# Optimization experiments

Measured on AMD Instinct MI355X. Metric: run time of the kernel, lower is better.

The kernel has to match this reference:

```python
import jax, jax.numpy as jnp
import numpy as np

N = 50000      # nodes
E = 800000     # edges
D_IN = 128     # input_dim
D = 128        # hidden_dim
H = 8          # num_heads
DH = D // H    # head dim
S = 10         # security_feature_dim
LN_EPS = 1e-5


def setup_inputs() -> dict:
    key = jax.random.key(0)
    ks = jax.random.split(key, 16)
    def lin_w(k, fin, fout):
        return (jax.random.normal(k, (fin, fout), jnp.float32) / np.sqrt(fin)).astype(jnp.float32)
    return {
        "x": jax.random.normal(ks[0], (N, D_IN), jnp.float32),
        "edge_index": jax.random.randint(ks[1], (2, E), 0, N, jnp.int64),
        "security_features": jax.random.normal(ks[2], (N, S), jnp.float32),
        "W1": lin_w(ks[3], D_IN, D), "b1": jnp.zeros((D,), jnp.float32),
        "W2": lin_w(ks[4], D, D),    "b2": jnp.zeros((D,), jnp.float32),
        "Wq": lin_w(ks[5], D, D),    "bq": jnp.zeros((D,), jnp.float32),
        "Wk": lin_w(ks[6], D, D),    "bk": jnp.zeros((D,), jnp.float32),
        "Wv": lin_w(ks[7], D, D),    "bv": jnp.zeros((D,), jnp.float32),
        "Wsec": lin_w(ks[8], S, H),  "bsec": jnp.zeros((H,), jnp.float32),
        "Wo": lin_w(ks[9], D, D),    "bo": jnp.zeros((D,), jnp.float32),
        "ln1_g": jnp.ones((D,), jnp.float32), "ln1_b": jnp.zeros((D,), jnp.float32),
        "ln2_g": jnp.ones((D,), jnp.float32), "ln2_b": jnp.zeros((D,), jnp.float32),
    }


def _layer_norm(x, g, b):
    m = jnp.mean(x, axis=-1, keepdims=True)
    v = jnp.mean(jnp.square(x - m), axis=-1, keepdims=True)
    return (x - m) * jax.lax.rsqrt(v + LN_EPS) * g + b


def reference(x, edge_index, security_features,
              W1, b1, W2, b2, Wq, bq, Wk, bk, Wv, bv,
              Wsec, bsec, Wo, bo, ln1_g, ln1_b, ln2_g, ln2_b):
    # h = relu(linear1(x))  -- [N, D]
    h = jax.nn.relu(x @ W1 + b1)

    # SecurityAwareAttention: edge-wise multi-head attention with a
    # per-edge security bias derived from the source node's security features.
    q = (h @ Wq + bq).reshape(N, H, DH)
    k = (h @ Wk + bk).reshape(N, H, DH)
    v = (h @ Wv + bv).reshape(N, H, DH)
    src, dst = edge_index[0], edge_index[1]

    sec_bias = security_features @ Wsec + bsec            # [N, H]
    scores = jnp.einsum('ehd,ehd->eh', q[dst], k[src]) / np.sqrt(DH) + sec_bias[src]  # [E, H]

    # segment softmax over incoming edges of each destination node
    m = jax.ops.segment_max(scores, dst, num_segments=N)  # [N, H]
    e = jnp.exp(scores - m[dst])
    s = jax.ops.segment_sum(e, dst, num_segments=N)       # [N, H]
    attn = e / (s[dst] + 1e-9)                            # [E, H]

    agg = jax.ops.segment_sum(attn[:, :, None] * v[src], dst, num_segments=N)  # [N, H, DH]
    attended = agg.reshape(N, D) @ Wo + bo

    # dropout is identity (eval mode)
    out = _layer_norm(h + attended, ln1_g, ln1_b)
    out = _layer_norm(out + jax.nn.relu(out @ W2 + b2), ln2_g, ln2_b)
    return (out, attn)
```

## Files before the change

### kernel.cpp

```cpp
#include <hip/hip_runtime.h>
#include <hip/hip_bf16.h>
#include <math.h>

#define N_NODES 50000
#define N_EDGES 800000
#define DIM 128
#define NHEAD 8
#define DHEAD 16
#define SDIM 10
#define NSCAN_BLK 196

typedef __attribute__((ext_vector_type(8))) short bf16x8;
typedef __attribute__((ext_vector_type(4))) float f32x4;

__device__ __forceinline__ float bf2f(unsigned short u) {
    return __uint_as_float(((unsigned)u) << 16);
}
__device__ __forceinline__ unsigned short f2bf(float f) {
    unsigned u = __float_as_uint(f);
    return (unsigned short)((u + 0x7FFFu + ((u >> 16) & 1u)) >> 16);
}

__global__ __launch_bounds__(256) void setup_kernel(
    const float* __restrict__ W1, const float* __restrict__ Wq,
    const float* __restrict__ Wk, const float* __restrict__ Wv,
    const float* __restrict__ Wo, const float* __restrict__ W2,
    unsigned short* __restrict__ Wt, int* __restrict__ deg, int* __restrict__ ctr,
    const float* __restrict__ sec, const float* __restrict__ Wsec,
    const float* __restrict__ bsec, float* __restrict__ secb) {
    const int b = blockIdx.x, t = threadIdx.x;
    if (b < 6) {
        const float* W = (b == 0) ? W1 : (b == 1) ? Wq : (b == 2) ? Wk :
                         (b == 3) ? Wv : (b == 4) ? Wo : W2;
        unsigned short* o = Wt + b * 16384;
        for (int i = 0; i < 64; ++i) {
            int idx = t + 256 * i;
            int k = idx >> 7, n = idx & 127;
            o[n * 128 + k] = f2bf(W[idx]);
        }
    } else if (b < 202) {
        int idx = (b - 6) * 256 + t;
        if (idx < N_NODES) { deg[idx] = 0; ctr[idx] = 0; }
    } else {
        int idx = (b - 202) * 256 + t;
        if (idx < N_NODES * NHEAD) {
            int n = idx >> 3, h = idx & 7;
            float acc = bsec[h];
#pragma unroll
            for (int j = 0; j < SDIM; ++j)
                acc = fmaf(sec[n * SDIM + j], Wsec[j * NHEAD + h], acc);
            secb[idx] = acc;
        }
    }
}

__global__ __launch_bounds__(256) void count_deg_kernel(const int* __restrict__ dst,
                                                        int* __restrict__ deg) {
    int e = blockIdx.x * 256 + threadIdx.x;
    if (e < N_EDGES) atomicAdd(&deg[dst[e]], 1);
}

__global__ __launch_bounds__(256) void blocksum_kernel(const int* __restrict__ deg,
                                                       int* __restrict__ bsum) {
    const int t = threadIdx.x;
    int idx = blockIdx.x * 256 + t;
    int v = (idx < N_NODES) ? deg[idx] : 0;
#pragma unroll
    for (int m = 32; m; m >>= 1) v += __shfl_xor(v, m);
    __shared__ int ws[4];
    if ((t & 63) == 0) ws[t >> 6] = v;
    __syncthreads();
    if (t == 0) bsum[blockIdx.x] = ws[0] + ws[1] + ws[2] + ws[3];
}

__global__ __launch_bounds__(256) void scanfin2_kernel(const int* __restrict__ deg,
                                                       const int* __restrict__ bsum,
                                                       int* __restrict__ rowstart) {
    const int t = threadIdx.x, b = blockIdx.x;
    int v0 = (t < b) ? bsum[t] : 0;
#pragma unroll
    for (int m = 32; m; m >>= 1) v0 += __shfl_xor(v0, m);
    __shared__ int ws[4];
    if ((t & 63) == 0) ws[t >> 6] = v0;
    __syncthreads();
    const int bexc = ws[0] + ws[1] + ws[2] + ws[3];

    int idx = b * 256 + t;
    int v = (idx < N_NODES) ? deg[idx] : 0;
    __shared__ int s[256];
    __syncthreads();
    s[t] = v;
    __syncthreads();
#pragma unroll
    for (int off = 1; off < 256; off <<= 1) {
        int x = (t >= off) ? s[t - off] : 0;
        __syncthreads();
        s[t] += x;
        __syncthreads();
    }
    if (idx < N_NODES) rowstart[idx] = bexc + s[t] - v;
    if (b == 0 && t == 0) rowstart[N_NODES] = N_EDGES;
}

__global__ __launch_bounds__(256) void fill_csr_kernel(
    const int* __restrict__ src, const int* __restrict__ dst,
    const int* __restrict__ rowstart, int* __restrict__ ctr,
    int* __restrict__ eidx, int* __restrict__ esrc) {
    int e = blockIdx.x * 256 + threadIdx.x;
    if (e >= N_EDGES) return;
    int d = dst[e];
    int pos = atomicAdd(&ctr[d], 1);
    int slot = rowstart[d] + pos;
    eidx[slot] = e;
    esrc[slot] = src[e];
}

__global__ __launch_bounds__(512) void gemm_hqkv_kernel(
    const float* __restrict__ X, const unsigned short* __restrict__ Wt,
    const float* __restrict__ b1, const float* __restrict__ bq,
    const float* __restrict__ bk, const float* __restrict__ bv,
    unsigned short* __restrict__ hb, unsigned short* __restrict__ qo,
    unsigned short* __restrict__ ko, unsigned short* __restrict__ vo, int nrows) {
    __shared__ alignas(16) unsigned char Wl[32768];
    __shared__ alignas(16) unsigned char Ht[32768];
    const int t = threadIdx.x;
    const int l = t & 63, wave = t >> 6;
    const int l15 = l & 15, lg = l >> 4;
    const int r0 = blockIdx.x * 128 + wave * 16;
    const int arow = r0 + l15;
    const bool aok = arow < nrows;
    const int orow0 = r0 + lg * 4;
    unsigned char* HtW = Ht + wave * 4096;

#pragma unroll
    for (int i = 0; i < 4; ++i) {
        int c = t + 512 * i;
        int n = c >> 4, s = c & 15;
        bf16x8 val = *(const bf16x8*)(Wt + c * 8);
        *(bf16x8*)(Wl + n * 256 + ((s * 16) ^ ((n & 7) << 4))) = val;
    }
    bf16x8 af[4];
#pragma unroll
    for (int k0 = 0; k0 < 4; ++k0) {
        float4 a0 = {0.f, 0.f, 0.f, 0.f}, a1 = {0.f, 0.f, 0.f, 0.f};
        if (aok) {
            const float4* ap = (const float4*)(X + (size_t)arow * DIM + k0 * 32 + lg * 8);
            a0 = ap[0]; a1 = ap[1];
        }
        bf16x8 f;
        f[0] = (short)f2bf(a0.x); f[1] = (short)f2bf(a0.y);
        f[2] = (short)f2bf(a0.z); f[3] = (short)f2bf(a0.w);
        f[4] = (short)f2bf(a1.x); f[5] = (short)f2bf(a1.y);
        f[6] = (short)f2bf(a1.z); f[7] = (short)f2bf(a1.w);
        af[k0] = f;
    }
    __syncthreads();

    {
        f32x4 acc[8];
#pragma unroll
        for (int n = 0; n < 8; ++n) acc[n] = (f32x4){0.f, 0.f, 0.f, 0.f};
#pragma unroll
        for (int k0 = 0; k0 < 4; ++k0) {
#pragma unroll
            for (int n = 0; n < 8; ++n) {
                int row = n * 16 + l15;
                int kb = (k0 * 64 + lg * 16) ^ ((row & 7) << 4);
                bf16x8 bfr = *(bf16x8*)(Wl + row * 256 + kb);
                acc[n] = __builtin_amdgcn_mfma_f32_16x16x32_bf16(af[k0], bfr, acc[n], 0, 0, 0);
            }
        }
#pragma unroll
        for (int n = 0; n < 8; ++n) {
            int col = n * 16 + l15;
            float bvv = b1[col];
#pragma unroll
            for (int i = 0; i < 4; ++i) {
                int rloc = lg * 4 + i;
                unsigned short hv = f2bf(fmaxf(acc[n][i] + bvv, 0.f));
                if (orow0 + i < nrows) hb[(size_t)(orow0 + i) * DIM + col] = hv;
                *(unsigned short*)(HtW + ((rloc * 256 + col * 2) ^ ((rloc & 7) << 4))) = hv;
            }
        }
    }
    __syncthreads();

    bf16x8 af2[4];
#pragma unroll
    for (int k0 = 0; k0 < 4; ++k0)
        af2[k0] = *(const bf16x8*)(HtW + ((l15 * 256 + k0 * 64 + lg * 16) ^ ((l15 & 7) << 4)));

    for (int m = 0; m < 3; ++m) {
        const unsigned short* wsrc = (m == 0) ? Wt + 16384 : (m == 1) ? Wt + 32768 : Wt + 49152;
        const float* bias = (m == 0) ? bq : (m == 1) ? bk : bv;
        unsigned short* outp = (m == 0) ? qo : (m == 1) ? ko : vo;
#pragma unroll
        for (int i = 0; i < 4; ++i) {
            int c = t + 512 * i;
            int n = c >> 4, s = c & 15;
            bf16x8 val = *(const bf16x8*)(wsrc + c * 8);
            *(bf16x8*)(Wl + n * 256 + ((s * 16) ^ ((n & 7) << 4))) = val;
        }
        __syncthreads();
        f32x4 acc[8];
#pragma unroll
        for (int n = 0; n < 8; ++n) acc[n] = (f32x4){0.f, 0.f, 0.f, 0.f};
#pragma unroll
        for (int k0 = 0; k0 < 4; ++k0) {
#pragma unroll
            for (int n = 0; n < 8; ++n) {
                int row = n * 16 + l15;
                int kb = (k0 * 64 + lg * 16) ^ ((row & 7) << 4);
                bf16x8 bfr = *(bf16x8*)(Wl + row * 256 + kb);
                acc[n] = __builtin_amdgcn_mfma_f32_16x16x32_bf16(af2[k0], bfr, acc[n], 0, 0, 0);
            }
        }
#pragma unroll
        for (int n = 0; n < 8; ++n) {
            int col = n * 16 + l15;
            float bvv = bias[col];
#pragma unroll
            for (int i = 0; i < 4; ++i) {
                int r = orow0 + i;
                if (r < nrows) outp[(size_t)r * DIM + col] = f2bf(acc[n][i] + bvv);
            }
        }
        __syncthreads();
    }
}

__global__ __launch_bounds__(256) void node_attn_kernel(
    const unsigned short* __restrict__ qb, const unsigned short* __restrict__ kb,
    const unsigned short* __restrict__ vb, const float* __restrict__ secb,
    const int* __restrict__ eidx, const int* __restrict__ esrc,
    const int* __restrict__ rowstart, float* __restrict__ attn_out,
    unsigned short* __restrict__ aggb) {
    int node = blockIdx.x * 4 + (threadIdx.x >> 6);
    if (node >= N_NODES) return;
    const int lane = threadIdx.x & 63;
    const int start = rowstart[node];
    const int deg = rowstart[node + 1] - start;
    if (deg == 0) {
        ((unsigned*)(aggb + (size_t)node * DIM))[lane] = 0u;
        return;
    }
    const int h = lane & 7;
    const int le = lane >> 3;
    const int hc = le;

    float qv[16];
    {
        const bf16x8* qp = (const bf16x8*)(qb + (size_t)node * DIM + h * DHEAD);
        bf16x8 q0 = qp[0], q1 = qp[1];
#pragma unroll
        for (int i = 0; i < 8; ++i) {
            qv[i] = bf2f((unsigned short)q0[i]);
            qv[8 + i] = bf2f((unsigned short)q1[i]);
        }
    }

    if (deg <= 64) {
        int sall = 0, eall = 0;
        if (lane < deg) {
            int idx = start + lane;
            sall = esrc[idx];
            eall = eidx[idx];
        }
        float sc[8];
        float m = -INFINITY;
#pragma unroll
        for (int t = 0; t < 8; ++t) {
            sc[t] = -INFINITY;
            if (t * 8 < deg) {
                int jj = t * 8 + le;
                bool valid = jj < deg;
                int s = __shfl(sall, valid ? jj : deg - 1);
                const bf16x8* kp = (const bf16x8*)(kb + (size_t)s * DIM + h * DHEAD);
                bf16x8 k0 = kp[0], k1 = kp[1];
                float acc = 0.f;
#pragma unroll
                for (int i = 0; i < 8; ++i) {
                    acc = fmaf(qv[i], bf2f((unsigned short)k0[i]), acc);
                    acc = fmaf(qv[8 + i], bf2f((unsigned short)k1[i]), acc);
                }
                if (valid) sc[t] = acc * 0.25f + secb[s * NHEAD + h];
            }
            m = fmaxf(m, sc[t]);
        }
        m = fmaxf(m, __shfl_xor(m, 8));
        m = fmaxf(m, __shfl_xor(m, 16));
        m = fmaxf(m, __shfl_xor(m, 32));

        float ev[8];
        float ssum = 0.f;
#pragma unroll
        for (int t = 0; t < 8; ++t) {
            ev[t] = (t * 8 + le < deg) ? __expf(sc[t] - m) : 0.f;
            ssum += ev[t];
        }
        ssum += __shfl_xor(ssum, 8);
        ssum += __shfl_xor(ssum, 16);
        ssum += __shfl_xor(ssum, 32);
        const float rinv = 1.f / (ssum + 1e-9f);

        float2 acc2 = {0.f, 0.f};
#pragma unroll
        for (int t = 0; t < 8; ++t) {
            if (t * 8 < deg) {
#pragma unroll
                for (int le2 = 0; le2 < 8; ++le2) {
                    int jj = t * 8 + le2;
                    int s = __shfl(sall, (jj < deg) ? jj : deg - 1);
                    float evd = __shfl(ev[t], le2 * 8 + hc);
                    unsigned vv = ((const unsigned*)(vb + (size_t)s * DIM))[lane];
                    acc2.x = fmaf(evd, bf2f((unsigned short)(vv & 0xFFFFu)), acc2.x);
                    acc2.y = fmaf(evd, bf2f((unsigned short)(vv >> 16)), acc2.y);
                }
            }
        }
        const float rinv_c = __shfl(rinv, hc);
        unsigned short o0 = f2bf(acc2.x * rinv_c);
        unsigned short o1 = f2bf(acc2.y * rinv_c);
        ((unsigned*)(aggb + (size_t)node * DIM))[lane] =
            (unsigned)o0 | ((unsigned)o1 << 16);

#pragma unroll
        for (int t = 0; t < 8; ++t) {
            int jj = t * 8 + le;
            int e = __shfl(eall, (jj < deg) ? jj : 0);
            if (jj < deg) attn_out[(size_t)e * NHEAD + h] = ev[t] * rinv;
        }
        return;
    }

    float m = -INFINITY;
    for (int j = 0; j < deg; j += 8) {
        int jj = j + le;
        float sc = -INFINITY;
        if (jj < deg) {
            int idx = start + jj;
            int s = esrc[idx];
            const bf16x8* kp = (const bf16x8*)(kb + (size_t)s * DIM + h * DHEAD);
            bf16x8 k0 = kp[0], k1 = kp[1];
            float acc = 0.f;
#pragma unroll
            for (int i = 0; i < 8; ++i) {
                acc = fmaf(qv[i], bf2f((unsigned short)k0[i]), acc);
                acc = fmaf(qv[8 + i], bf2f((unsigned short)k1[i]), acc);
            }
            sc = acc * 0.25f + secb[s * NHEAD + h];
            int e = eidx[idx];
            attn_out[(size_t)e * NHEAD + h] = sc;
        }
        m = fmaxf(m, sc);
    }
    m = fmaxf(m, __shfl_xor(m, 8));
    m = fmaxf(m, __shfl_xor(m, 16));
    m = fmaxf(m, __shfl_xor(m, 32));

    float ssum = 0.f;
    float2 acc2 = {0.f, 0.f};
    for (int j = 0; j < deg; j += 8) {
        int jj = j + le;
        float ev = 0.f;
        if (jj < deg) {
            int e = eidx[start + jj];
            ev = __expf(attn_out[(size_t)e * NHEAD + h] - m);
        }
        ssum += ev;
        int lim = deg - j; if (lim > 8) lim = 8;
        for (int le2 = 0; le2 < lim; ++le2) {
            float evd = __shfl(ev, le2 * 8 + hc);
            int s = esrc[start + j + le2];
            unsigned vv = ((const unsigned*)(vb + (size_t)s * DIM))[lane];
            acc2.x = fmaf(evd, bf2f((unsigned short)(vv & 0xFFFFu)), acc2.x);
            acc2.y = fmaf(evd, bf2f((unsigned short)(vv >> 16)), acc2.y);
        }
    }
    ssum += __shfl_xor(ssum, 8);
    ssum += __shfl_xor(ssum, 16);
    ssum += __shfl_xor(ssum, 32);
    const float rinv = 1.f / (ssum + 1e-9f);
    const float rinv_c = __shfl(rinv, hc);

    unsigned short o0 = f2bf(acc2.x * rinv_c);
    unsigned short o1 = f2bf(acc2.y * rinv_c);
    ((unsigned*)(aggb + (size_t)node * DIM))[lane] =
        (unsigned)o0 | ((unsigned)o1 << 16);

    for (int j = 0; j < deg; j += 8) {
        int jj = j + le;
        if (jj < deg) {
            int e = eidx[start + jj];
            float sc = attn_out[(size_t)e * NHEAD + h];
            attn_out[(size_t)e * NHEAD + h] = __expf(sc - m) * rinv;
        }
    }
}

__global__ __launch_bounds__(512) void gemm_ln12_kernel(
    const unsigned short* __restrict__ A,
    const unsigned short* __restrict__ Wt,
    const float* __restrict__ bo, const float* __restrict__ b2,
    const unsigned short* __restrict__ resid,
    const float* __restrict__ g1, const float* __restrict__ be1,
    const float* __restrict__ g2, const float* __restrict__ be2,
    float* __restrict__ outp, int nrows) {
    __shared__ alignas(16) unsigned char Wl[32768];
    __shared__ alignas(16) unsigned char Mt[32768];
    const int t = threadIdx.x;
    const int l = t & 63, wave = t >> 6;
    const int l15 = l & 15, lg = l >> 4;
    const int r0 = blockIdx.x * 128 + wave * 16;
    const int arow = r0 + l15;
    const bool aok = arow < nrows;
    const int orow0 = r0 + lg * 4;
    unsigned char* MtW = Mt + wave * 4096;

#pragma unroll
    for (int i = 0; i < 4; ++i) {
        int c = t + 512 * i;
        int n = c >> 4, s = c & 15;
        bf16x8 val = *(const bf16x8*)(Wt + c * 8);
        *(bf16x8*)(Wl + n * 256 + ((s * 16) ^ ((n & 7) << 4))) = val;
    }
    bf16x8 af[4];
#pragma unroll
    for (int k0 = 0; k0 < 4; ++k0) {
        bf16x8 z = (bf16x8){0, 0, 0, 0, 0, 0, 0, 0};
        af[k0] = aok ? *(const bf16x8*)(A + (size_t)arow * DIM + k0 * 32 + lg * 8) : z;
    }
    __syncthreads();

    float mid[8][4];
    {
        f32x4 acc[8];
#pragma unroll
        for (int n = 0; n < 8; ++n) acc[n] = (f32x4){0.f, 0.f, 0.f, 0.f};
#pragma unroll
        for (int k0 = 0; k0 < 4; ++k0) {
#pragma unroll
            for (int n = 0; n < 8; ++n) {
                int row = n * 16 + l15;
                int kb = (k0 * 64 + lg * 16) ^ ((row & 7) << 4);
                bf16x8 bfr = *(bf16x8*)(Wl + row * 256 + kb);
                acc[n] = __builtin_amdgcn_mfma_f32_16x16x32_bf16(af[k0], bfr, acc[n], 0, 0, 0);
            }
        }
        float bv[8], gv[8], bev[8];
#pragma unroll
        for (int n = 0; n < 8; ++n) {
            int col = n * 16 + l15;
            bv[n] = bo[col]; gv[n] = g1[col]; bev[n] = be1[col];
        }
#pragma unroll
        for (int i = 0; i < 4; ++i) {
            int r = orow0 + i;
            int rloc = lg * 4 + i;
            float xv[8];
            float s = 0.f;
            if (r < nrows) {
#pragma unroll
                for (int n = 0; n < 8; ++n) {
                    float val = acc[n][i] + bv[n]
                              + bf2f(resid[(size_t)r * DIM + n * 16 + l15]);
                    xv[n] = val;
                    s += val;
                }
            } else {
#pragma unroll
                for (int n = 0; n < 8; ++n) xv[n] = 0.f;
            }
            s += __shfl_xor(s, 1); s += __shfl_xor(s, 2);
            s += __shfl_xor(s, 4); s += __shfl_xor(s, 8);
            float mean = s * (1.f / 128.f);
            float var = 0.f;
#pragma unroll
            for (int n = 0; n < 8; ++n) {
                float d = xv[n] - mean;
                var += d * d;
            }
            var += __shfl_xor(var, 1); var += __shfl_xor(var, 2);
            var += __shfl_xor(var, 4); var += __shfl_xor(var, 8);
            float rstd = rsqrtf(var * (1.f / 128.f) + 1e-5f);
#pragma unroll
            for (int n = 0; n < 8; ++n) {
                int col = n * 16 + l15;
                unsigned short mb = f2bf((xv[n] - mean) * rstd * gv[n] + bev[n]);
                mid[n][i] = bf2f(mb);
                *(unsigned short*)(MtW + ((rloc * 256 + col * 2) ^ ((rloc & 7) << 4))) = mb;
            }
        }
    }
    __syncthreads();

    bf16x8 af2[4];
#pragma unroll
    for (int k0 = 0; k0 < 4; ++k0)
        af2[k0] = *(const bf16x8*)(MtW + ((l15 * 256 + k0 * 64 + lg * 16) ^ ((l15 & 7) << 4)));

#pragma unroll
    for (int i = 0; i < 4; ++i) {
        int c = t + 512 * i;
        int n = c >> 4, s = c & 15;
        bf16x8 val = *(const bf16x8*)(Wt + 16384 + c * 8);
        *(bf16x8*)(Wl + n * 256 + ((s * 16) ^ ((n & 7) << 4))) = val;
    }
    __syncthreads();

    {
        f32x4 acc[8];
#pragma unroll
        for (int n = 0; n < 8; ++n) acc[n] = (f32x4){0.f, 0.f, 0.f, 0.f};
#pragma unroll
        for (int k0 = 0; k0 < 4; ++k0) {
#pragma unroll
            for (int n = 0; n < 8; ++n) {
                int row = n * 16 + l15;
                int kb = (k0 * 64 + lg * 16) ^ ((row & 7) << 4);
                bf16x8 bfr = *(bf16x8*)(Wl + row * 256 + kb);
                acc[n] = __builtin_amdgcn_mfma_f32_16x16x32_bf16(af2[k0], bfr, acc[n], 0, 0, 0);
            }
        }
        float bv[8], gv[8], bev[8];
#pragma unroll
        for (int n = 0; n < 8; ++n) {
            int col = n * 16 + l15;
            bv[n] = b2[col]; gv[n] = g2[col]; bev[n] = be2[col];
        }
#pragma unroll
        for (int i = 0; i < 4; ++i) {
            int r = orow0 + i;
            float xv[8];
            float s = 0.f;
#pragma unroll
            for (int n = 0; n < 8; ++n) {
                float val = fmaxf(acc[n][i] + bv[n], 0.f) + mid[n][i];
                xv[n] = val;
                s += val;
            }
            s += __shfl_xor(s, 1); s += __shfl_xor(s, 2);
            s += __shfl_xor(s, 4); s += __shfl_xor(s, 8);
            float mean = s * (1.f / 128.f);
            float var = 0.f;
#pragma unroll
            for (int n = 0; n < 8; ++n) {
                float d = xv[n] - mean;
                var += d * d;
            }
            var += __shfl_xor(var, 1); var += __shfl_xor(var, 2);
            var += __shfl_xor(var, 4); var += __shfl_xor(var, 8);
            float rstd = rsqrtf(var * (1.f / 128.f) + 1e-5f);
            if (r < nrows) {
#pragma unroll
                for (int n = 0; n < 8; ++n) {
                    int col = n * 16 + l15;
                    outp[(size_t)r * DIM + col] = (xv[n] - mean) * rstd * gv[n] + bev[n];
                }
            }
        }
    }
}

extern "C" void kernel_launch(void* const* d_in, const int* in_sizes, int n_in,
                              void* d_out, int out_size, void* d_ws, size_t ws_size,
                              hipStream_t stream) {
    const float* x    = (const float*)d_in[0];
    const int*   ei   = (const int*)d_in[1];
    const float* sec  = (const float*)d_in[2];
    const float* W1   = (const float*)d_in[3];
    const float* b1   = (const float*)d_in[4];
    const float* W2   = (const float*)d_in[5];
    const float* b2   = (const float*)d_in[6];
    const float* Wq   = (const float*)d_in[7];
    const float* bq   = (const float*)d_in[8];
    const float* Wk   = (const float*)d_in[9];
    const float* bk   = (const float*)d_in[10];
    const float* Wv   = (const float*)d_in[11];
    const float* bvp  = (const float*)d_in[12];
    const float* Wsec = (const float*)d_in[13];
    const float* bsec = (const float*)d_in[14];
    const float* Wo   = (const float*)d_in[15];
    const float* bo   = (const float*)d_in[16];
    const float* g1   = (const float*)d_in[17];
    const float* be1  = (const float*)d_in[18];
    const float* g2   = (const float*)d_in[19];
    const float* be2  = (const float*)d_in[20];

    const int* srcp = ei;
    const int* dstp = ei + N_EDGES;

    char* wsb = (char*)d_ws;
    unsigned short* hb   = (unsigned short*)(wsb);
    unsigned short* qbu  = (unsigned short*)(wsb + 12800000);
    unsigned short* kbu  = (unsigned short*)(wsb + 25600000);
    unsigned short* vbu  = (unsigned short*)(wsb + 38400000);
    unsigned short* aggb = (unsigned short*)(wsb + 51200000);
    float* secb          = (float*)(wsb + 76800000);
    unsigned short* Wt   = (unsigned short*)(wsb + 78400000);
    int* deg             = (int*)(wsb + 78600000);
    int* ctr             = (int*)(wsb + 78800000);
    int* rowstart        = (int*)(wsb + 79000000);
    int* eidxb           = (int*)(wsb + 79200256);
    int* esrcb           = (int*)(wsb + 82400256);
    int* bsum            = (int*)(wsb + 85600256);

    float* outp = (float*)d_out;
    float* attn = outp + (size_t)N_NODES * DIM;

    dim3 blk(256);
    const int big_grid = (N_NODES + 127) / 128;
    const int egrid = (N_EDGES + 255) / 256;
    const int wgrid = (N_NODES + 3) / 4;

    setup_kernel<<<6 + 196 + 1563, blk, 0, stream>>>(W1, Wq, Wk, Wv, Wo, W2, Wt,
                                                     deg, ctr, sec, Wsec, bsec, secb);
    count_deg_kernel<<<egrid, blk, 0, stream>>>(dstp, deg);
    blocksum_kernel<<<NSCAN_BLK, blk, 0, stream>>>(deg, bsum);
    scanfin2_kernel<<<NSCAN_BLK, blk, 0, stream>>>(deg, bsum, rowstart);
    fill_csr_kernel<<<egrid, blk, 0, stream>>>(srcp, dstp, rowstart, ctr, eidxb, esrcb);

    gemm_hqkv_kernel<<<big_grid, dim3(512), 0, stream>>>(x, Wt, b1, bq, bk, bvp,
                                                         hb, qbu, kbu, vbu, N_NODES);

    node_attn_kernel<<<wgrid, blk, 0, stream>>>(qbu, kbu, vbu, secb, eidxb, esrcb,
                                                rowstart, attn, aggb);

    gemm_ln12_kernel<<<big_grid, dim3(512), 0, stream>>>(aggb, Wt + 65536, bo, b2, hb,
                                                         g1, be1, g2, be2, outp, N_NODES);
}
```

Baseline: 224.3 us.

## Fuse degree counting into setup, pack CSR src/eid pairs, memset counters

```diff
diff --git a/kernel.cpp b/kernel.cpp
--- a/kernel.cpp
+++ b/kernel.cpp
@@ -9,6 +9,9 @@
 #define DHEAD 16
 #define SDIM 10
 #define NSCAN_BLK 196
+#define SETUP_W 48
+#define SETUP_CNT 3125
+#define SETUP_SEC 1563
 
 typedef __attribute__((ext_vector_type(8))) short bf16x8;
 typedef __attribute__((ext_vector_type(4))) float f32x4;
@@ -25,24 +28,27 @@
     const float* __restrict__ W1, const float* __restrict__ Wq,
     const float* __restrict__ Wk, const float* __restrict__ Wv,
     const float* __restrict__ Wo, const float* __restrict__ W2,
-    unsigned short* __restrict__ Wt, int* __restrict__ deg, int* __restrict__ ctr,
-    const float* __restrict__ sec, const float* __restrict__ Wsec,
-    const float* __restrict__ bsec, float* __restrict__ secb) {
+    unsigned short* __restrict__ Wt, const int* __restrict__ dst,
+    int* __restrict__ deg, const float* __restrict__ sec,
+    const float* __restrict__ Wsec, const float* __restrict__ bsec,
+    float* __restrict__ secb) {
     const int b = blockIdx.x, t = threadIdx.x;
-    if (b < 6) {
-        const float* W = (b == 0) ? W1 : (b == 1) ? Wq : (b == 2) ? Wk :
-                         (b == 3) ? Wv : (b == 4) ? Wo : W2;
-        unsigned short* o = Wt + b * 16384;
-        for (int i = 0; i < 64; ++i) {
-            int idx = t + 256 * i;
+    if (b < SETUP_W) {
+        const int mtx = b >> 3, slice = b & 7;
+        const float* W = (mtx == 0) ? W1 : (mtx == 1) ? Wq : (mtx == 2) ? Wk :
+                         (mtx == 3) ? Wv : (mtx == 4) ? Wo : W2;
+        unsigned short* o = Wt + mtx * 16384;
+#pragma unroll
+        for (int i = 0; i < 8; ++i) {
+            int idx = slice * 2048 + t + 256 * i;
             int k = idx >> 7, n = idx & 127;
             o[n * 128 + k] = f2bf(W[idx]);
         }
-    } else if (b < 202) {
-        int idx = (b - 6) * 256 + t;
-        if (idx < N_NODES) { deg[idx] = 0; ctr[idx] = 0; }
+    } else if (b < SETUP_W + SETUP_CNT) {
+        int e = (b - SETUP_W) * 256 + t;
+        if (e < N_EDGES) atomicAdd(&deg[dst[e]], 1);
     } else {
-        int idx = (b - 202) * 256 + t;
+        int idx = (b - SETUP_W - SETUP_CNT) * 256 + t;
         if (idx < N_NODES * NHEAD) {
             int n = idx >> 3, h = idx & 7;
             float acc = bsec[h];
@@ -52,12 +58,6 @@
             secb[idx] = acc;
         }
     }
-}
-
-__global__ __launch_bounds__(256) void count_deg_kernel(const int* __restrict__ dst,
-                                                        int* __restrict__ deg) {
-    int e = blockIdx.x * 256 + threadIdx.x;
-    if (e < N_EDGES) atomicAdd(&deg[dst[e]], 1);
 }
 
 __global__ __launch_bounds__(256) void blocksum_kernel(const int* __restrict__ deg,
@@ -105,14 +105,12 @@
 __global__ __launch_bounds__(256) void fill_csr_kernel(
     const int* __restrict__ src, const int* __restrict__ dst,
     const int* __restrict__ rowstart, int* __restrict__ ctr,
-    int* __restrict__ eidx, int* __restrict__ esrc) {
+    int2* __restrict__ epair) {
     int e = blockIdx.x * 256 + threadIdx.x;
     if (e >= N_EDGES) return;
     int d = dst[e];
     int pos = atomicAdd(&ctr[d], 1);
-    int slot = rowstart[d] + pos;
-    eidx[slot] = e;
-    esrc[slot] = src[e];
+    epair[rowstart[d] + pos] = make_int2(src[e], e);
 }
 
 __global__ __launch_bounds__(512) void gemm_hqkv_kernel(
@@ -232,9 +230,8 @@
 __global__ __launch_bounds__(256) void node_attn_kernel(
     const unsigned short* __restrict__ qb, const unsigned short* __restrict__ kb,
     const unsigned short* __restrict__ vb, const float* __restrict__ secb,
-    const int* __restrict__ eidx, const int* __restrict__ esrc,
-    const int* __restrict__ rowstart, float* __restrict__ attn_out,
-    unsigned short* __restrict__ aggb) {
+    const int2* __restrict__ epair, const int* __restrict__ rowstart,
+    float* __restrict__ attn_out, unsigned short* __restrict__ aggb) {
     int node = blockIdx.x * 4 + (threadIdx.x >> 6);
     if (node >= N_NODES) return;
     const int lane = threadIdx.x & 63;
@@ -262,9 +259,9 @@
     if (deg <= 64) {
         int sall = 0, eall = 0;
         if (lane < deg) {
-            int idx = start + lane;
-            sall = esrc[idx];
-            eall = eidx[idx];
+            int2 p = epair[start + lane];
+            sall = p.x;
+            eall = p.y;
         }
         float sc[8];
         float m = -INFINITY;
@@ -338,8 +335,8 @@
         int jj = j + le;
         float sc = -INFINITY;
         if (jj < deg) {
-            int idx = start + jj;
-            int s = esrc[idx];
+            int2 p = epair[start + jj];
+            int s = p.x;
             const bf16x8* kp = (const bf16x8*)(kb + (size_t)s * DIM + h * DHEAD);
             bf16x8 k0 = kp[0], k1 = kp[1];
             float acc = 0.f;
@@ -349,8 +346,7 @@
                 acc = fmaf(qv[8 + i], bf2f((unsigned short)k1[i]), acc);
             }
             sc = acc * 0.25f + secb[s * NHEAD + h];
-            int e = eidx[idx];
-            attn_out[(size_t)e * NHEAD + h] = sc;
+            attn_out[(size_t)p.y * NHEAD + h] = sc;
         }
         m = fmaxf(m, sc);
     }
@@ -364,14 +360,14 @@
         int jj = j + le;
         float ev = 0.f;
         if (jj < deg) {
-            int e = eidx[start + jj];
+            int e = epair[start + jj].y;
             ev = __expf(attn_out[(size_t)e * NHEAD + h] - m);
         }
         ssum += ev;
         int lim = deg - j; if (lim > 8) lim = 8;
         for (int le2 = 0; le2 < lim; ++le2) {
             float evd = __shfl(ev, le2 * 8 + hc);
-            int s = esrc[start + j + le2];
+            int s = epair[start + j + le2].x;
             unsigned vv = ((const unsigned*)(vb + (size_t)s * DIM))[lane];
             acc2.x = fmaf(evd, bf2f((unsigned short)(vv & 0xFFFFu)), acc2.x);
             acc2.y = fmaf(evd, bf2f((unsigned short)(vv >> 16)), acc2.y);
@@ -391,7 +387,7 @@
     for (int j = 0; j < deg; j += 8) {
         int jj = j + le;
         if (jj < deg) {
-            int e = eidx[start + jj];
+            int e = epair[start + jj].y;
             float sc = attn_out[(size_t)e * NHEAD + h];
             attn_out[(size_t)e * NHEAD + h] = __expf(sc - m) * rinv;
         }
@@ -601,9 +597,8 @@
     int* deg             = (int*)(wsb + 78600000);
     int* ctr             = (int*)(wsb + 78800000);
     int* rowstart        = (int*)(wsb + 79000000);
-    int* eidxb           = (int*)(wsb + 79200256);
-    int* esrcb           = (int*)(wsb + 82400256);
-    int* bsum            = (int*)(wsb + 85600256);
+    int2* epair          = (int2*)(wsb + 79200256);
+    int* bsum            = (int*)(wsb + 85600512);
 
     float* outp = (float*)d_out;
     float* attn = outp + (size_t)N_NODES * DIM;
@@ -613,17 +608,18 @@
     const int egrid = (N_EDGES + 255) / 256;
     const int wgrid = (N_NODES + 3) / 4;
 
-    setup_kernel<<<6 + 196 + 1563, blk, 0, stream>>>(W1, Wq, Wk, Wv, Wo, W2, Wt,
-                                                     deg, ctr, sec, Wsec, bsec, secb);
-    count_deg_kernel<<<egrid, blk, 0, stream>>>(dstp, deg);
+    hipMemsetAsync(deg, 0, 400000, stream);
+
+    setup_kernel<<<SETUP_W + SETUP_CNT + SETUP_SEC, blk, 0, stream>>>(
+        W1, Wq, Wk, Wv, Wo, W2, Wt, dstp, deg, sec, Wsec, bsec, secb);
     blocksum_kernel<<<NSCAN_BLK, blk, 0, stream>>>(deg, bsum);
     scanfin2_kernel<<<NSCAN_BLK, blk, 0, stream>>>(deg, bsum, rowstart);
-    fill_csr_kernel<<<egrid, blk, 0, stream>>>(srcp, dstp, rowstart, ctr, eidxb, esrcb);
+    fill_csr_kernel<<<egrid, blk, 0, stream>>>(srcp, dstp, rowstart, ctr, epair);
 
     gemm_hqkv_kernel<<<big_grid, dim3(512), 0, stream>>>(x, Wt, b1, bq, bk, bvp,
                                                          hb, qbu, kbu, vbu, N_NODES);
 
-    node_attn_kernel<<<wgrid, blk, 0, stream>>>(qbu, kbu, vbu, secb, eidxb, esrcb,
+    node_attn_kernel<<<wgrid, blk, 0, stream>>>(qbu, kbu, vbu, secb, epair,
                                                 rowstart, attn, aggb);
 
     gemm_ln12_kernel<<<big_grid, dim3(512), 0, stream>>>(aggb, Wt + 65536, bo, b2, hb,
```

After: 216.6 us. 3.4% less time.
